# Kernel optimization log

Measured on AMD Instinct MI355X. Metric: run time of the kernel, lower is better.

The kernel has to match this reference:

```python
import jax, jax.numpy as jnp
import numpy as np

H = 4096  # hidden_size
B, S = 4, 2048
LN_EPS = 1e-5


def setup_inputs() -> dict:
    key = jax.random.key(0)
    ks = jax.random.split(key, 8)
    return {
        "x": jax.random.normal(ks[0], (B, S, H), dtype=jnp.float32),
        "ln_gamma": jnp.ones((H,), dtype=jnp.float32),
        "ln_beta": jnp.zeros((H,), dtype=jnp.float32),
        "w_mu": jax.random.normal(ks[1], (H, H), dtype=jnp.float32) * 0.02,
        "w_rho": jax.random.normal(ks[2], (H, H), dtype=jnp.float32) * 0.1,  # posterior_rho_init=0.0, std 0.1
        "b_mu": jax.random.normal(ks[3], (H,), dtype=jnp.float32) * 0.02,
        "b_rho": jax.random.normal(ks[4], (H,), dtype=jnp.float32) * 0.1,
        "eps_w": jax.random.normal(ks[5], (H, H), dtype=jnp.float32),
        "eps_b": jax.random.normal(ks[6], (H,), dtype=jnp.float32),
    }


def reference(x, ln_gamma, ln_beta, w_mu, w_rho, b_mu, b_rho, eps_w, eps_b):
    residual = x
    # LayerNorm over last dim
    mean = jnp.mean(x, axis=-1, keepdims=True)
    var = jnp.var(x, axis=-1, keepdims=True)
    h = (x - mean) * jax.lax.rsqrt(var + LN_EPS) * ln_gamma + ln_beta
    # Bayesian reparameterized linear: W = mu + softplus(rho) * eps
    W = w_mu + jax.nn.softplus(w_rho) * eps_w            # [H_out, H_in]
    b = b_mu + jax.nn.softplus(b_rho) * eps_b            # [H_out]
    y = jnp.einsum("bsh,oh->bso", h, W) + b
    # exact (erf) GELU, matching torch.nn.functional.gelu default
    y = jax.nn.gelu(y, approximate=False)
    return residual + y
```

## Files before the change

kernel.cpp:

```cpp
#include <hip/hip_runtime.h>
#include <hip/hip_bf16.h>
#include <cstdint>
#include <cstddef>

#define HDIM 4096
#define MROWS 8192
#define LN_EPS 1e-5f

typedef __bf16 bf16_t;
typedef __bf16 bf16x4_t __attribute__((ext_vector_type(4)));
typedef __bf16 bf16x8_t __attribute__((ext_vector_type(8)));
typedef float f32x4_t __attribute__((ext_vector_type(4)));

typedef const __attribute__((address_space(1))) void gvoid_t;
typedef __attribute__((address_space(3))) void lvoid_t;

__device__ __forceinline__ float softplus_f(float x) {
    return fmaxf(x, 0.f) + log1pf(expf(-fabsf(x)));
}

__global__ __launch_bounds__(256) void wgen_kernel(
    const float* __restrict__ mu, const float* __restrict__ rho,
    const float* __restrict__ eps, bf16_t* __restrict__ W)
{
    int i = (blockIdx.x * 256 + threadIdx.x) * 4;
    float4 m = *(const float4*)(mu + i);
    float4 r = *(const float4*)(rho + i);
    float4 e = *(const float4*)(eps + i);
    bf16x4_t o;
    o[0] = (bf16_t)(m.x + softplus_f(r.x) * e.x);
    o[1] = (bf16_t)(m.y + softplus_f(r.y) * e.y);
    o[2] = (bf16_t)(m.z + softplus_f(r.z) * e.z);
    o[3] = (bf16_t)(m.w + softplus_f(r.w) * e.w);
    *(bf16x4_t*)(W + i) = o;
}

__global__ __launch_bounds__(256) void biasgen_kernel(
    const float* __restrict__ mu, const float* __restrict__ rho,
    const float* __restrict__ eps, float* __restrict__ b)
{
    int i = blockIdx.x * 256 + threadIdx.x;
    b[i] = mu[i] + softplus_f(rho[i]) * eps[i];
}

__global__ __launch_bounds__(256) void ln_kernel(
    const float* __restrict__ x, const float* __restrict__ gamma,
    const float* __restrict__ beta, bf16_t* __restrict__ h)
{
    int row = blockIdx.x;
    const float* xr = x + (size_t)row * HDIM;
    int t = threadIdx.x;
    float4 v[4];
    float s = 0.f, s2 = 0.f;
#pragma unroll
    for (int j = 0; j < 4; ++j) {
        v[j] = *(const float4*)(xr + j * 1024 + t * 4);
        s  += v[j].x + v[j].y + v[j].z + v[j].w;
        s2 += v[j].x * v[j].x + v[j].y * v[j].y + v[j].z * v[j].z + v[j].w * v[j].w;
    }
#pragma unroll
    for (int off = 32; off > 0; off >>= 1) {
        s  += __shfl_down(s, off);
        s2 += __shfl_down(s2, off);
    }
    __shared__ float ps[4], ps2[4];
    if ((t & 63) == 0) { ps[t >> 6] = s; ps2[t >> 6] = s2; }
    __syncthreads();
    float tot  = ps[0] + ps[1] + ps[2] + ps[3];
    float tot2 = ps2[0] + ps2[1] + ps2[2] + ps2[3];
    float mean = tot * (1.f / HDIM);
    float var  = tot2 * (1.f / HDIM) - mean * mean;
    float rstd = rsqrtf(var + LN_EPS);
    bf16_t* hr = h + (size_t)row * HDIM;
#pragma unroll
    for (int j = 0; j < 4; ++j) {
        int c = j * 1024 + t * 4;
        float4 g  = *(const float4*)(gamma + c);
        float4 bb = *(const float4*)(beta + c);
        bf16x4_t o;
        o[0] = (bf16_t)((v[j].x - mean) * rstd * g.x + bb.x);
        o[1] = (bf16_t)((v[j].y - mean) * rstd * g.y + bb.y);
        o[2] = (bf16_t)((v[j].z - mean) * rstd * g.z + bb.z);
        o[3] = (bf16_t)((v[j].w - mean) * rstd * g.w + bb.w);
        *(bf16x4_t*)(hr + c) = o;
    }
}

__device__ __forceinline__ void gload_lds16(const bf16_t* g, const char* l) {
    __builtin_amdgcn_global_load_lds((gvoid_t*)g, (lvoid_t*)l, 16, 0, 0);
}

__device__ __forceinline__ int swz(int x) { return x ^ ((x >> 3) & 0x30); }

__global__ __launch_bounds__(512, 2) void gemm_kernel(
    const bf16_t* __restrict__ A,
    const bf16_t* __restrict__ B,
    const float* __restrict__ bias,
    const float* __restrict__ xres,
    float* __restrict__ out)
{
    __shared__ char lds[131072];

    const int tid  = threadIdx.x;
    const int lane = tid & 63, w = tid >> 6;
    const int g = lane >> 4, fr = lane & 15;
    const int wm = w >> 2, wn = w & 3;

    int bid = blockIdx.x;
    int wg  = (bid & 7) * 64 + (bid >> 3);
    const int tileN = (wg & 15) * 256;
    const int tileM = (wg >> 4) * 256;

    const bf16_t* srcA[2];
    const bf16_t* srcB[2];
    int ldstA[2], ldstB[2];
#pragma unroll
    for (int r = 0; r < 2; ++r) {
        int D = r * 8192 + w * 1024 + lane * 16;
        int S = swz(D);
        int row = S >> 6, colel = (S & 63) >> 1;
        srcA[r] = A + (size_t)(tileM + row) * HDIM + colel;
        srcB[r] = B + (size_t)(tileN + row) * HDIM + colel;
        ldstA[r] = r * 8192 + w * 1024;
        ldstB[r] = 16384 + r * 8192 + w * 1024;
    }

    int aoff[8], boff[4];
#pragma unroll
    for (int m = 0; m < 8; ++m)
        aoff[m] = swz(wm * 8192 + m * 1024 + fr * 64 + g * 16);
#pragma unroll
    for (int n = 0; n < 4; ++n)
        boff[n] = 16384 + swz(wn * 4096 + n * 1024 + fr * 64 + g * 16);

    f32x4_t acc[8][4] = {};
    const int NT = HDIM / 32;

#define STAGE(bb, kofs)                                          \
    do {                                                         \
        gload_lds16(srcA[0] + (kofs), &lds[(bb) + ldstA[0]]);    \
        gload_lds16(srcA[1] + (kofs), &lds[(bb) + ldstA[1]]);    \
        gload_lds16(srcB[0] + (kofs), &lds[(bb) + ldstB[0]]);    \
        gload_lds16(srcB[1] + (kofs), &lds[(bb) + ldstB[1]]);    \
    } while (0)

    STAGE(0, 0);
    STAGE(32768, 32);
    STAGE(65536, 64);
    asm volatile("s_waitcnt vmcnt(8)" ::: "memory");
    __builtin_amdgcn_s_barrier();
    __builtin_amdgcn_sched_barrier(0);

#pragma unroll 1
    for (int t = 0; t < NT; ++t) {
        int ts = (t + 3) & (NT - 1);
        STAGE(((t + 3) & 3) * 32768, ts * 32);

        const char* buf = &lds[(t & 3) * 32768];
        bf16x8_t af[8], bv[4];
#pragma unroll
        for (int m = 0; m < 8; ++m)
            af[m] = *(const bf16x8_t*)(buf + aoff[m]);
#pragma unroll
        for (int n = 0; n < 4; ++n)
            bv[n] = *(const bf16x8_t*)(buf + boff[n]);

        __builtin_amdgcn_s_setprio(1);
#pragma unroll
        for (int m = 0; m < 8; ++m)
#pragma unroll
            for (int n = 0; n < 4; ++n)
                acc[m][n] = __builtin_amdgcn_mfma_f32_16x16x32_bf16(
                    af[m], bv[n], acc[m][n], 0, 0, 0);
        __builtin_amdgcn_s_setprio(0);

        asm volatile("s_waitcnt lgkmcnt(0)" ::: "memory");
        asm volatile("s_waitcnt vmcnt(8)" ::: "memory");
        __builtin_amdgcn_s_barrier();
        __builtin_amdgcn_sched_barrier(0);
    }
#undef STAGE

    const int col0 = tileN + wn * 64 + fr;
    const int row0 = tileM + wm * 128 + g * 4;
#pragma unroll
    for (int n = 0; n < 4; ++n) {
        float bvv = bias[col0 + n * 16];
#pragma unroll
        for (int m = 0; m < 8; ++m) {
#pragma unroll
            for (int j = 0; j < 4; ++j) {
                size_t idx = (size_t)(row0 + m * 16 + j) * HDIM + (col0 + n * 16);
                float v = acc[m][n][j] + bvv;
                float ge = 0.5f * v * (1.0f + erff(v * 0.70710678118654752f));
                out[idx] = xres[idx] + ge;
            }
        }
    }
}

extern "C" void kernel_launch(void* const* d_in, const int* in_sizes, int n_in,
                              void* d_out, int out_size, void* d_ws, size_t ws_size,
                              hipStream_t stream) {
    const float* x        = (const float*)d_in[0];
    const float* ln_gamma = (const float*)d_in[1];
    const float* ln_beta  = (const float*)d_in[2];
    const float* w_mu     = (const float*)d_in[3];
    const float* w_rho    = (const float*)d_in[4];
    const float* b_mu     = (const float*)d_in[5];
    const float* b_rho    = (const float*)d_in[6];
    const float* eps_w    = (const float*)d_in[7];
    const float* eps_b    = (const float*)d_in[8];
    float* out = (float*)d_out;

    char* ws = (char*)d_ws;
    bf16_t* h_bf16 = (bf16_t*)ws;
    bf16_t* W_bf16 = (bf16_t*)(ws + 67108864);
    float*  bias   = (float*)(ws + 67108864 + 33554432);

    wgen_kernel<<<16384, 256, 0, stream>>>(w_mu, w_rho, eps_w, W_bf16);
    biasgen_kernel<<<16, 256, 0, stream>>>(b_mu, b_rho, eps_b, bias);
    ln_kernel<<<MROWS, 256, 0, stream>>>(x, ln_gamma, ln_beta, h_bf16);
    gemm_kernel<<<512, 512, 0, stream>>>(h_bf16, W_bf16, bias, x, out);
}
```

Before: 440.3 us.

## Split GEMM main loop into two interleaved phases of LDS reads, loads and MFMAs

Restructures each K-iteration of the GEMM into two halves. Each half reads part of the A fragments from LDS, issues half of the next stage's global-to-LDS loads (A first, then B), synchronises and runs 16 MFMAs. The aim is to interleave memory issue with MFMA work in the ping-pong style used by hand-tuned AMD kernels and to reduce register pressure from holding all fragments at once. It adds two extra workgroup barriers per iteration, which may cost more than the overlap gains.

```diff
diff --git a/kernel.cpp b/kernel.cpp
--- a/kernel.cpp
+++ b/kernel.cpp
@@ -136,42 +136,87 @@
     f32x4_t acc[8][4] = {};
     const int NT = HDIM / 32;
 
-#define STAGE(bb, kofs)                                          \
+#define STAGE_A(bb, kofs)                                        \
     do {                                                         \
         gload_lds16(srcA[0] + (kofs), &lds[(bb) + ldstA[0]]);    \
         gload_lds16(srcA[1] + (kofs), &lds[(bb) + ldstA[1]]);    \
+    } while (0)
+#define STAGE_B(bb, kofs)                                        \
+    do {                                                         \
         gload_lds16(srcB[0] + (kofs), &lds[(bb) + ldstB[0]]);    \
         gload_lds16(srcB[1] + (kofs), &lds[(bb) + ldstB[1]]);    \
     } while (0)
 
-    STAGE(0, 0);
-    STAGE(32768, 32);
-    STAGE(65536, 64);
+    STAGE_A(0, 0);      STAGE_B(0, 0);
+    STAGE_A(32768, 32); STAGE_B(32768, 32);
+    STAGE_A(65536, 64); STAGE_B(65536, 64);
     asm volatile("s_waitcnt vmcnt(8)" ::: "memory");
     __builtin_amdgcn_s_barrier();
     __builtin_amdgcn_sched_barrier(0);
 
 #pragma unroll 1
     for (int t = 0; t < NT; ++t) {
-        int ts = (t + 3) & (NT - 1);
-        STAGE(((t + 3) & 3) * 32768, ts * 32);
-
         const char* buf = &lds[(t & 3) * 32768];
-        bf16x8_t af[8], bv[4];
-#pragma unroll
-        for (int m = 0; m < 8; ++m)
-            af[m] = *(const bf16x8_t*)(buf + aoff[m]);
-#pragma unroll
-        for (int n = 0; n < 4; ++n)
-            bv[n] = *(const bf16x8_t*)(buf + boff[n]);
-
+        const int sb = ((t + 3) & 3) * 32768;
+        const int sk = ((t + 3) & (NT - 1)) * 32;
+
+        bf16x8_t af0, af1, af2, af3, bv0, bv1, bv2, bv3;
+        af0 = *(const bf16x8_t*)(buf + aoff[0]);
+        af1 = *(const bf16x8_t*)(buf + aoff[1]);
+        af2 = *(const bf16x8_t*)(buf + aoff[2]);
+        af3 = *(const bf16x8_t*)(buf + aoff[3]);
+        bv0 = *(const bf16x8_t*)(buf + boff[0]);
+        bv1 = *(const bf16x8_t*)(buf + boff[1]);
+        bv2 = *(const bf16x8_t*)(buf + boff[2]);
+        bv3 = *(const bf16x8_t*)(buf + boff[3]);
+        STAGE_A(sb, sk);
+        __builtin_amdgcn_s_barrier();
+        __builtin_amdgcn_sched_barrier(0);
         __builtin_amdgcn_s_setprio(1);
-#pragma unroll
-        for (int m = 0; m < 8; ++m)
-#pragma unroll
-            for (int n = 0; n < 4; ++n)
-                acc[m][n] = __builtin_amdgcn_mfma_f32_16x16x32_bf16(
-                    af[m], bv[n], acc[m][n], 0, 0, 0);
+        acc[0][0] = __builtin_amdgcn_mfma_f32_16x16x32_bf16(af0, bv0, acc[0][0], 0, 0, 0);
+        acc[0][1] = __builtin_amdgcn_mfma_f32_16x16x32_bf16(af0, bv1, acc[0][1], 0, 0, 0);
+        acc[0][2] = __builtin_amdgcn_mfma_f32_16x16x32_bf16(af0, bv2, acc[0][2], 0, 0, 0);
+        acc[0][3] = __builtin_amdgcn_mfma_f32_16x16x32_bf16(af0, bv3, acc[0][3], 0, 0, 0);
+        acc[1][0] = __builtin_amdgcn_mfma_f32_16x16x32_bf16(af1, bv0, acc[1][0], 0, 0, 0);
+        acc[1][1] = __builtin_amdgcn_mfma_f32_16x16x32_bf16(af1, bv1, acc[1][1], 0, 0, 0);
+        acc[1][2] = __builtin_amdgcn_mfma_f32_16x16x32_bf16(af1, bv2, acc[1][2], 0, 0, 0);
+        acc[1][3] = __builtin_amdgcn_mfma_f32_16x16x32_bf16(af1, bv3, acc[1][3], 0, 0, 0);
+        acc[2][0] = __builtin_amdgcn_mfma_f32_16x16x32_bf16(af2, bv0, acc[2][0], 0, 0, 0);
+        acc[2][1] = __builtin_amdgcn_mfma_f32_16x16x32_bf16(af2, bv1, acc[2][1], 0, 0, 0);
+        acc[2][2] = __builtin_amdgcn_mfma_f32_16x16x32_bf16(af2, bv2, acc[2][2], 0, 0, 0);
+        acc[2][3] = __builtin_amdgcn_mfma_f32_16x16x32_bf16(af2, bv3, acc[2][3], 0, 0, 0);
+        acc[3][0] = __builtin_amdgcn_mfma_f32_16x16x32_bf16(af3, bv0, acc[3][0], 0, 0, 0);
+        acc[3][1] = __builtin_amdgcn_mfma_f32_16x16x32_bf16(af3, bv1, acc[3][1], 0, 0, 0);
+        acc[3][2] = __builtin_amdgcn_mfma_f32_16x16x32_bf16(af3, bv2, acc[3][2], 0, 0, 0);
+        acc[3][3] = __builtin_amdgcn_mfma_f32_16x16x32_bf16(af3, bv3, acc[3][3], 0, 0, 0);
+        __builtin_amdgcn_s_setprio(0);
+        __builtin_amdgcn_sched_barrier(0);
+
+        bf16x8_t af4, af5, af6, af7;
+        af4 = *(const bf16x8_t*)(buf + aoff[4]);
+        af5 = *(const bf16x8_t*)(buf + aoff[5]);
+        af6 = *(const bf16x8_t*)(buf + aoff[6]);
+        af7 = *(const bf16x8_t*)(buf + aoff[7]);
+        STAGE_B(sb, sk);
+        __builtin_amdgcn_s_barrier();
+        __builtin_amdgcn_sched_barrier(0);
+        __builtin_amdgcn_s_setprio(1);
+        acc[4][0] = __builtin_amdgcn_mfma_f32_16x16x32_bf16(af4, bv0, acc[4][0], 0, 0, 0);
+        acc[4][1] = __builtin_amdgcn_mfma_f32_16x16x32_bf16(af4, bv1, acc[4][1], 0, 0, 0);
+        acc[4][2] = __builtin_amdgcn_mfma_f32_16x16x32_bf16(af4, bv2, acc[4][2], 0, 0, 0);
+        acc[4][3] = __builtin_amdgcn_mfma_f32_16x16x32_bf16(af4, bv3, acc[4][3], 0, 0, 0);
+        acc[5][0] = __builtin_amdgcn_mfma_f32_16x16x32_bf16(af5, bv0, acc[5][0], 0, 0, 0);
+        acc[5][1] = __builtin_amdgcn_mfma_f32_16x16x32_bf16(af5, bv1, acc[5][1], 0, 0, 0);
+        acc[5][2] = __builtin_amdgcn_mfma_f32_16x16x32_bf16(af5, bv2, acc[5][2], 0, 0, 0);
+        acc[5][3] = __builtin_amdgcn_mfma_f32_16x16x32_bf16(af5, bv3, acc[5][3], 0, 0, 0);
+        acc[6][0] = __builtin_amdgcn_mfma_f32_16x16x32_bf16(af6, bv0, acc[6][0], 0, 0, 0);
+        acc[6][1] = __builtin_amdgcn_mfma_f32_16x16x32_bf16(af6, bv1, acc[6][1], 0, 0, 0);
+        acc[6][2] = __builtin_amdgcn_mfma_f32_16x16x32_bf16(af6, bv2, acc[6][2], 0, 0, 0);
+        acc[6][3] = __builtin_amdgcn_mfma_f32_16x16x32_bf16(af6, bv3, acc[6][3], 0, 0, 0);
+        acc[7][0] = __builtin_amdgcn_mfma_f32_16x16x32_bf16(af7, bv0, acc[7][0], 0, 0, 0);
+        acc[7][1] = __builtin_amdgcn_mfma_f32_16x16x32_bf16(af7, bv1, acc[7][1], 0, 0, 0);
+        acc[7][2] = __builtin_amdgcn_mfma_f32_16x16x32_bf16(af7, bv2, acc[7][2], 0, 0, 0);
+        acc[7][3] = __builtin_amdgcn_mfma_f32_16x16x32_bf16(af7, bv3, acc[7][3], 0, 0, 0);
         __builtin_amdgcn_s_setprio(0);
 
         asm volatile("s_waitcnt lgkmcnt(0)" ::: "memory");
@@ -179,7 +224,8 @@
         __builtin_amdgcn_s_barrier();
         __builtin_amdgcn_sched_barrier(0);
     }
-#undef STAGE
+#undef STAGE_A
+#undef STAGE_B
 
     const int col0 = tileN + wn * 64 + fr;
     const int row0 = tileM + wm * 128 + g * 4;
```

Result: faster. 430.3 us (-2.3%).

## Software-pipeline LDS fragment reads with MFMA via two-phase ping-pong B registers

Applied to the files above, without the earlier changes.

Splits each K-step into two phases separated by barriers: half the A fragments are read while the other half are fed to MFMAs, and the next tile's B fragments are prefetched into alternate register sets. Global-to-LDS staging is also split into A and B halves across the phases. The goal is to hide LDS read latency behind matrix instructions instead of waiting on lgkmcnt(0) before computing. It doubles the barrier count, uses more registers for the double-buffered B fragments, and adds a tighter vmcnt wait pattern that has to stay correct across the four-buffer ring.

```diff
diff --git a/kernel.cpp b/kernel.cpp
--- a/kernel.cpp
+++ b/kernel.cpp
@@ -136,50 +136,86 @@
     f32x4_t acc[8][4] = {};
     const int NT = HDIM / 32;
 
-#define STAGE(bb, kofs)                                          \
+    bf16x8_t af0, af1, af2, af3, af4, af5, af6, af7;
+    bf16x8_t bvA0, bvA1, bvA2, bvA3, bvB0, bvB1, bvB2, bvB3;
+
+#define STAGE_A(bb, kofs)                                        \
     do {                                                         \
         gload_lds16(srcA[0] + (kofs), &lds[(bb) + ldstA[0]]);    \
         gload_lds16(srcA[1] + (kofs), &lds[(bb) + ldstA[1]]);    \
+    } while (0)
+#define STAGE_B(bb, kofs)                                        \
+    do {                                                         \
         gload_lds16(srcB[0] + (kofs), &lds[(bb) + ldstB[0]]);    \
         gload_lds16(srcB[1] + (kofs), &lds[(bb) + ldstB[1]]);    \
     } while (0)
-
-    STAGE(0, 0);
-    STAGE(32768, 32);
-    STAGE(65536, 64);
+#define RD_SET1(bp)                                  \
+    af4 = *(const bf16x8_t*)((bp) + aoff[4]);        \
+    af5 = *(const bf16x8_t*)((bp) + aoff[5]);        \
+    af6 = *(const bf16x8_t*)((bp) + aoff[6]);        \
+    af7 = *(const bf16x8_t*)((bp) + aoff[7]);
+#define RD_SET0(bp, V)                               \
+    af0 = *(const bf16x8_t*)((bp) + aoff[0]);        \
+    af1 = *(const bf16x8_t*)((bp) + aoff[1]);        \
+    af2 = *(const bf16x8_t*)((bp) + aoff[2]);        \
+    af3 = *(const bf16x8_t*)((bp) + aoff[3]);        \
+    V##0 = *(const bf16x8_t*)((bp) + boff[0]);       \
+    V##1 = *(const bf16x8_t*)((bp) + boff[1]);       \
+    V##2 = *(const bf16x8_t*)((bp) + boff[2]);       \
+    V##3 = *(const bf16x8_t*)((bp) + boff[3]);
+#define CL(AF, V, R)                                                            \
+    acc[R][0] = __builtin_amdgcn_mfma_f32_16x16x32_bf16(AF, V##0, acc[R][0], 0, 0, 0); \
+    acc[R][1] = __builtin_amdgcn_mfma_f32_16x16x32_bf16(AF, V##1, acc[R][1], 0, 0, 0); \
+    acc[R][2] = __builtin_amdgcn_mfma_f32_16x16x32_bf16(AF, V##2, acc[R][2], 0, 0, 0); \
+    acc[R][3] = __builtin_amdgcn_mfma_f32_16x16x32_bf16(AF, V##3, acc[R][3], 0, 0, 0);
+#define SCHEDB __builtin_amdgcn_sched_barrier(0)
+#define BARRIER do { __builtin_amdgcn_s_barrier(); SCHEDB; } while (0)
+#define VMCNT6 do { asm volatile("s_waitcnt vmcnt(6)" ::: "memory"); SCHEDB; } while (0)
+
+#define PHASE_X(tc, V)                                               \
+    do {                                                             \
+        BARRIER;                                                     \
+        const char* bp_ = &lds[((tc) & 3) * 32768];                  \
+        RD_SET1(bp_);                                                \
+        STAGE_A((((tc) + 3) & 3) * 32768, (((tc) + 3) & (NT - 1)) * 32); \
+        SCHEDB;                                                      \
+        __builtin_amdgcn_s_setprio(1);                               \
+        CL(af0, V, 0) CL(af1, V, 1) CL(af2, V, 2) CL(af3, V, 3)      \
+        __builtin_amdgcn_s_setprio(0);                               \
+        SCHEDB;                                                      \
+        VMCNT6;                                                      \
+    } while (0)
+#define PHASE_Y(tc, Vnext, Vcur)                                     \
+    do {                                                             \
+        BARRIER;                                                     \
+        const char* bp_ = &lds[(((tc) + 1) & 3) * 32768];            \
+        RD_SET0(bp_, Vnext);                                         \
+        STAGE_B((((tc) + 3) & 3) * 32768, (((tc) + 3) & (NT - 1)) * 32); \
+        SCHEDB;                                                      \
+        __builtin_amdgcn_s_setprio(1);                               \
+        CL(af4, Vcur, 4) CL(af5, Vcur, 5) CL(af6, Vcur, 6) CL(af7, Vcur, 7) \
+        __builtin_amdgcn_s_setprio(0);                               \
+        SCHEDB;                                                      \
+    } while (0)
+
+    STAGE_A(0, 0);      STAGE_B(0, 0);
+    STAGE_A(32768, 32); STAGE_B(32768, 32);
+    STAGE_A(65536, 64); STAGE_B(65536, 64);
     asm volatile("s_waitcnt vmcnt(8)" ::: "memory");
-    __builtin_amdgcn_s_barrier();
-    __builtin_amdgcn_sched_barrier(0);
+    BARRIER;
+    RD_SET0(&lds[0], bvA);
 
 #pragma unroll 1
-    for (int t = 0; t < NT; ++t) {
-        int ts = (t + 3) & (NT - 1);
-        STAGE(((t + 3) & 3) * 32768, ts * 32);
-
-        const char* buf = &lds[(t & 3) * 32768];
-        bf16x8_t af[8], bv[4];
-#pragma unroll
-        for (int m = 0; m < 8; ++m)
-            af[m] = *(const bf16x8_t*)(buf + aoff[m]);
-#pragma unroll
-        for (int n = 0; n < 4; ++n)
-            bv[n] = *(const bf16x8_t*)(buf + boff[n]);
-
-        __builtin_amdgcn_s_setprio(1);
-#pragma unroll
-        for (int m = 0; m < 8; ++m)
-#pragma unroll
-            for (int n = 0; n < 4; ++n)
-                acc[m][n] = __builtin_amdgcn_mfma_f32_16x16x32_bf16(
-                    af[m], bv[n], acc[m][n], 0, 0, 0);
-        __builtin_amdgcn_s_setprio(0);
-
-        asm volatile("s_waitcnt lgkmcnt(0)" ::: "memory");
-        asm volatile("s_waitcnt vmcnt(8)" ::: "memory");
-        __builtin_amdgcn_s_barrier();
-        __builtin_amdgcn_sched_barrier(0);
-    }
-#undef STAGE
+    for (int t = 0; t < NT; t += 2) {
+        PHASE_X(t, bvA);
+        PHASE_Y(t, bvB, bvA);
+        PHASE_X(t + 1, bvB);
+        PHASE_Y(t + 1, bvA, bvB);
+    }
+#undef PHASE_X
+#undef PHASE_Y
+#undef STAGE_A
+#undef STAGE_B
 
     const int col0 = tileN + wn * 64 + fr;
     const int row0 = tileM + wm * 128 + g * 4;
```

New measurement: 425.9 us. -3.3%, faster.

## Split GEMM k-step into two half-phases interleaving LDS reads, global staging, and MFMA

Applied to the files above, without the earlier changes.

Each k-iteration of the GEMM main loop is split into two phases. The first reads half the A fragments plus all B fragments and issues the A-tile prefetch, then runs 16 MFMAs. The second reads the other half of A and issues the B-tile prefetch, then runs the remaining 16 MFMAs. LDS reads now use raw inline ds_read_b128, and an extra barrier sits between the phases. The intent is to spread global-to-LDS traffic and LDS reads across the MFMA work, in the style of ping-pong scheduling, at the cost of one more barrier per iteration and fewer live A fragment registers.

```diff
diff --git a/kernel.cpp b/kernel.cpp
--- a/kernel.cpp
+++ b/kernel.cpp
@@ -90,6 +90,12 @@
     __builtin_amdgcn_global_load_lds((gvoid_t*)g, (lvoid_t*)l, 16, 0, 0);
 }
 
+__device__ __forceinline__ bf16x8_t ds_read_b128_raw(const char* p) {
+    f32x4_t r;
+    asm volatile("ds_read_b128 %0, %1" : "=v"(r) : "v"((lvoid_t*)p));
+    return __builtin_bit_cast(bf16x8_t, r);
+}
+
 __device__ __forceinline__ int swz(int x) { return x ^ ((x >> 3) & 0x30); }
 
 __global__ __launch_bounds__(512, 2) void gemm_kernel(
@@ -136,50 +142,74 @@
     f32x4_t acc[8][4] = {};
     const int NT = HDIM / 32;
 
-#define STAGE(bb, kofs)                                          \
+    bf16x8_t af0, af1, af2, af3, af4, af5, af6, af7;
+    bf16x8_t bv0, bv1, bv2, bv3;
+
+#define STAGE_A(bb, kofs)                                        \
     do {                                                         \
         gload_lds16(srcA[0] + (kofs), &lds[(bb) + ldstA[0]]);    \
         gload_lds16(srcA[1] + (kofs), &lds[(bb) + ldstA[1]]);    \
+    } while (0)
+#define STAGE_B(bb, kofs)                                        \
+    do {                                                         \
         gload_lds16(srcB[0] + (kofs), &lds[(bb) + ldstB[0]]);    \
         gload_lds16(srcB[1] + (kofs), &lds[(bb) + ldstB[1]]);    \
     } while (0)
-
-    STAGE(0, 0);
-    STAGE(32768, 32);
-    STAGE(65536, 64);
+#define CL(AF, R)                                                               \
+    acc[R][0] = __builtin_amdgcn_mfma_f32_16x16x32_bf16(AF, bv0, acc[R][0], 0, 0, 0); \
+    acc[R][1] = __builtin_amdgcn_mfma_f32_16x16x32_bf16(AF, bv1, acc[R][1], 0, 0, 0); \
+    acc[R][2] = __builtin_amdgcn_mfma_f32_16x16x32_bf16(AF, bv2, acc[R][2], 0, 0, 0); \
+    acc[R][3] = __builtin_amdgcn_mfma_f32_16x16x32_bf16(AF, bv3, acc[R][3], 0, 0, 0);
+#define SCHEDB __builtin_amdgcn_sched_barrier(0)
+#define BARRIER do { __builtin_amdgcn_s_barrier(); SCHEDB; } while (0)
+#define LGKM0 do { asm volatile("s_waitcnt lgkmcnt(0)" ::: "memory"); SCHEDB; } while (0)
+#define VMCNT8 do { asm volatile("s_waitcnt vmcnt(8)" ::: "memory"); SCHEDB; } while (0)
+
+    STAGE_A(0, 0);      STAGE_B(0, 0);
+    STAGE_A(32768, 32); STAGE_B(32768, 32);
+    STAGE_A(65536, 64); STAGE_B(65536, 64);
     asm volatile("s_waitcnt vmcnt(8)" ::: "memory");
-    __builtin_amdgcn_s_barrier();
-    __builtin_amdgcn_sched_barrier(0);
+    BARRIER;
 
 #pragma unroll 1
     for (int t = 0; t < NT; ++t) {
-        int ts = (t + 3) & (NT - 1);
-        STAGE(((t + 3) & 3) * 32768, ts * 32);
-
         const char* buf = &lds[(t & 3) * 32768];
-        bf16x8_t af[8], bv[4];
-#pragma unroll
-        for (int m = 0; m < 8; ++m)
-            af[m] = *(const bf16x8_t*)(buf + aoff[m]);
-#pragma unroll
-        for (int n = 0; n < 4; ++n)
-            bv[n] = *(const bf16x8_t*)(buf + boff[n]);
-
+        const int sb = ((t + 3) & 3) * 32768;
+        const int sk = ((t + 3) & (NT - 1)) * 32;
+
+        af0 = ds_read_b128_raw(buf + aoff[0]);
+        af1 = ds_read_b128_raw(buf + aoff[1]);
+        af2 = ds_read_b128_raw(buf + aoff[2]);
+        af3 = ds_read_b128_raw(buf + aoff[3]);
+        bv0 = ds_read_b128_raw(buf + boff[0]);
+        bv1 = ds_read_b128_raw(buf + boff[1]);
+        bv2 = ds_read_b128_raw(buf + boff[2]);
+        bv3 = ds_read_b128_raw(buf + boff[3]);
+        STAGE_A(sb, sk);
+        SCHEDB;
+        LGKM0;
         __builtin_amdgcn_s_setprio(1);
-#pragma unroll
-        for (int m = 0; m < 8; ++m)
-#pragma unroll
-            for (int n = 0; n < 4; ++n)
-                acc[m][n] = __builtin_amdgcn_mfma_f32_16x16x32_bf16(
-                    af[m], bv[n], acc[m][n], 0, 0, 0);
+        CL(af0, 0) CL(af1, 1) CL(af2, 2) CL(af3, 3)
         __builtin_amdgcn_s_setprio(0);
-
-        asm volatile("s_waitcnt lgkmcnt(0)" ::: "memory");
-        asm volatile("s_waitcnt vmcnt(8)" ::: "memory");
-        __builtin_amdgcn_s_barrier();
-        __builtin_amdgcn_sched_barrier(0);
-    }
-#undef STAGE
+        SCHEDB;
+        BARRIER;
+
+        af4 = ds_read_b128_raw(buf + aoff[4]);
+        af5 = ds_read_b128_raw(buf + aoff[5]);
+        af6 = ds_read_b128_raw(buf + aoff[6]);
+        af7 = ds_read_b128_raw(buf + aoff[7]);
+        STAGE_B(sb, sk);
+        SCHEDB;
+        LGKM0;
+        __builtin_amdgcn_s_setprio(1);
+        CL(af4, 4) CL(af5, 5) CL(af6, 6) CL(af7, 7)
+        __builtin_amdgcn_s_setprio(0);
+        SCHEDB;
+        VMCNT8;
+        BARRIER;
+    }
+#undef STAGE_A
+#undef STAGE_B
 
     const int col0 = tileN + wn * 64 + fr;
     const int row0 = tileM + wm * 128 + g * 4;
```

Measured after the change: 428.8 us. -2.6%, faster.
